# Kernel optimization log

Hardware: AMD Instinct MI355X
Metric: run time of the kernel (lower is better)

The kernel has to match this reference:

```python
import jax, jax.numpy as jnp
import numpy as np

B = 65536
BASE_CW = 0.5  # constraint weight at epoch 0 (progress=0)

def setup_inputs() -> dict:
    key = jax.random.key(0)
    k1, k2 = jax.random.split(key)
    outputs = jax.random.normal(k1, (B, 81, 9), dtype=jnp.float32)
    targets = jax.random.randint(k2, (B, 81), 0, 9, dtype=jnp.int64)
    return {"outputs": outputs, "targets": targets}

def reference(outputs, targets):
    b = outputs.shape[0]
    # log-softmax over the 9 digit classes (single stable pass)
    logp = jax.nn.log_softmax(outputs, axis=2)            # (B, 81, 9)
    t = targets.reshape(-1)                               # (B*81,)
    # cross entropy (mean over all cells)
    ce = -jnp.take_along_axis(logp.reshape(-1, 9), t[:, None], axis=1).mean()
    probs = jnp.exp(logp)                                 # softmax probs
    grid = probs.reshape(b, 9, 9, 9)                      # (B, row, col, digit)
    # all 27 constraint MSEs fused: per-digit mean over (B, 9), summed over digits
    row_sums = grid.sum(axis=2)                           # (B, 9, 9)
    col_sums = grid.sum(axis=1)                           # (B, 9, 9)
    box_sums = grid.reshape(b, 3, 3, 3, 3, 9).sum(axis=(2, 4)).reshape(b, 9, 9)
    constraint_loss = (
        jnp.mean((row_sums - 1.0) ** 2, axis=(0, 1)).sum()
        + jnp.mean((col_sums - 1.0) ** 2, axis=(0, 1)).sum()
        + jnp.mean((box_sums - 1.0) ** 2, axis=(0, 1)).sum()
    ) / 27.0
    # confidence (entropy) term, masked by targets != -1
    mask = (t != -1).astype(outputs.dtype)                # (B*81,)
    conf = -(probs.reshape(-1, 9) * logp.reshape(-1, 9)).sum(axis=1)
    conf = (conf * mask).sum() / (mask.sum() + 1e-8)
    return ce + BASE_CW * constraint_loss + 0.1 * conf
```

## Files before the change

### kernel.cpp

```cpp
#include <hip/hip_runtime.h>

#define THREADS 256
#define BPB 8

static __global__ void zero_out_kernel(float* out) { out[0] = 0.0f; }

__launch_bounds__(THREADS)
static __global__ void sudoku_loss_kernel(const float* __restrict__ outs,
                                          const int*   __restrict__ targets,
                                          float*       __restrict__ out) {
    __shared__ float P[BPB * 729];
    __shared__ float wave_sums[THREADS / 64];

    const int tid = threadIdx.x;
    const long long board0 = (long long)blockIdx.x * BPB;
    const long long fbase  = board0 * 729;

    const float4* __restrict__ src = (const float4*)(outs + fbase);
    float4* dst = (float4*)P;
    for (int i = tid; i < (BPB * 729 / 4); i += THREADS) dst[i] = src[i];
    __syncthreads();

    float acc_a = 0.0f;
    const long long cbase = board0 * 81;
    for (int cell = tid; cell < BPB * 81; cell += THREADS) {
        const int t = targets[cbase + cell];
        float* xp = &P[cell * 9];
        float x[9];
        #pragma unroll
        for (int i = 0; i < 9; ++i) x[i] = xp[i];
        float m = x[0];
        #pragma unroll
        for (int i = 1; i < 9; ++i) m = fmaxf(m, x[i]);
        float s = 0.0f, sx = 0.0f, xt = 0.0f;
        float e[9];
        #pragma unroll
        for (int i = 0; i < 9; ++i) {
            e[i] = __expf(x[i] - m);
            s += e[i];
            sx = fmaf(e[i], x[i], sx);
            xt = (i == t) ? x[i] : xt;
        }
        const float lse = m + __logf(s);
        const float inv = 1.0f / s;
        const float ce  = lse - xt;
        const float ent = lse - sx * inv;
        acc_a += ce + 0.1f * ent;
        #pragma unroll
        for (int i = 0; i < 9; ++i) xp[i] = e[i] * inv;
    }
    __syncthreads();

    float acc_c = 0.0f;
    for (int u = tid; u < BPB * 243; u += THREADS) {
        const int q    = u / 243;
        const int r    = u - q * 243;
        const int type = r / 81;
        const int rem  = r - type * 81;
        const int unit = rem / 9;
        const int d    = rem - unit * 9;
        const float* Pq = &P[q * 729 + d];
        float ssum = 0.0f;
        if (type == 0) {
            #pragma unroll
            for (int j = 0; j < 9; ++j) ssum += Pq[(unit * 9 + j) * 9];
        } else if (type == 1) {
            #pragma unroll
            for (int j = 0; j < 9; ++j) ssum += Pq[(j * 9 + unit) * 9];
        } else {
            const int br = unit / 3, bc = unit - br * 3;
            #pragma unroll
            for (int j = 0; j < 9; ++j) {
                const int jr = j / 3, jc = j - jr * 3;
                ssum += Pq[((br * 3 + jr) * 9 + (bc * 3 + jc)) * 9];
            }
        }
        const float dlt = ssum - 1.0f;
        acc_c = fmaf(dlt, dlt, acc_c);
    }

    const float SA = 1.0f / (65536.0f * 81.0f);
    const float SB = 0.5f / (27.0f * 65536.0f * 9.0f);
    float total = acc_a * SA + acc_c * SB;
    #pragma unroll
    for (int off = 32; off > 0; off >>= 1)
        total += __shfl_down(total, off, 64);
    if ((tid & 63) == 0) wave_sums[tid >> 6] = total;
    __syncthreads();
    if (tid == 0) {
        float blk = wave_sums[0] + wave_sums[1] + wave_sums[2] + wave_sums[3];
        atomicAdd(out, blk);
    }
}

extern "C" void kernel_launch(void* const* d_in, const int* in_sizes, int n_in,
                              void* d_out, int out_size, void* d_ws, size_t ws_size,
                              hipStream_t stream) {
    const float* outs    = (const float*)d_in[0];
    const int*   targets = (const int*)d_in[1];
    float*       out     = (float*)d_out;
    hipLaunchKernelGGL(zero_out_kernel, dim3(1), dim3(1), 0, stream, out);
    hipLaunchKernelGGL(sudoku_loss_kernel, dim3(65536 / BPB), dim3(THREADS), 0, stream,
                       outs, targets, out);
}
```

Measured before the change: 336.3 us.

## Read logits directly from global and pad shared prob layout for vector reads

Drops the staging copy of logits into shared memory, so each thread loads its cell's 9 logits directly from global. Probabilities are written into a padded shared layout (12 floats per cell) using float4 stores. The constraint stage is remapped so each of 216 threads owns one (board, unit) pair and sums all 9 digits with float4 loads, instead of one thread per digit doing strided scalar reads. The risks are uncoalesced global loads, since each thread reads 36 contiguous bytes at a 36-byte stride, and fewer active threads in the constraint stage.

```diff
diff --git a/kernel.cpp b/kernel.cpp
--- a/kernel.cpp
+++ b/kernel.cpp
@@ -2,6 +2,8 @@
 
 #define THREADS 256
 #define BPB 8
+#define CELLS (BPB * 81)
+#define PADW 12
 
 static __global__ void zero_out_kernel(float* out) { out[0] = 0.0f; }
 
@@ -9,26 +11,22 @@
 static __global__ void sudoku_loss_kernel(const float* __restrict__ outs,
                                           const int*   __restrict__ targets,
                                           float*       __restrict__ out) {
-    __shared__ float P[BPB * 729];
+    __shared__ float P[CELLS * PADW];
     __shared__ float wave_sums[THREADS / 64];
 
     const int tid = threadIdx.x;
     const long long board0 = (long long)blockIdx.x * BPB;
-    const long long fbase  = board0 * 729;
-
-    const float4* __restrict__ src = (const float4*)(outs + fbase);
-    float4* dst = (float4*)P;
-    for (int i = tid; i < (BPB * 729 / 4); i += THREADS) dst[i] = src[i];
-    __syncthreads();
+    const float* __restrict__ xbase = outs + board0 * 729;
+    const int*   __restrict__ tbase = targets + board0 * 81;
 
     float acc_a = 0.0f;
-    const long long cbase = board0 * 81;
-    for (int cell = tid; cell < BPB * 81; cell += THREADS) {
-        const int t = targets[cbase + cell];
-        float* xp = &P[cell * 9];
+    for (int cell = tid; cell < CELLS; cell += THREADS) {
+        const float* __restrict__ xp = xbase + cell * 9;
+        const int t = tbase[cell];
         float x[9];
         #pragma unroll
         for (int i = 0; i < 9; ++i) x[i] = xp[i];
+
         float m = x[0];
         #pragma unroll
         for (int i = 1; i < 9; ++i) m = fmaxf(m, x[i]);
@@ -43,40 +41,48 @@
         }
         const float lse = m + __logf(s);
         const float inv = 1.0f / s;
-        const float ce  = lse - xt;
-        const float ent = lse - sx * inv;
-        acc_a += ce + 0.1f * ent;
-        #pragma unroll
-        for (int i = 0; i < 9; ++i) xp[i] = e[i] * inv;
+        acc_a += (lse - xt) + 0.1f * (lse - sx * inv);
+
+        float* __restrict__ pp = &P[cell * PADW];
+        float4 p0, p1;
+        p0.x = e[0] * inv; p0.y = e[1] * inv; p0.z = e[2] * inv; p0.w = e[3] * inv;
+        p1.x = e[4] * inv; p1.y = e[5] * inv; p1.z = e[6] * inv; p1.w = e[7] * inv;
+        *(float4*)pp       = p0;
+        *(float4*)(pp + 4) = p1;
+        pp[8] = e[8] * inv;
     }
     __syncthreads();
 
     float acc_c = 0.0f;
-    for (int u = tid; u < BPB * 243; u += THREADS) {
-        const int q    = u / 243;
-        const int r    = u - q * 243;
-        const int type = r / 81;
-        const int rem  = r - type * 81;
-        const int unit = rem / 9;
-        const int d    = rem - unit * 9;
-        const float* Pq = &P[q * 729 + d];
-        float ssum = 0.0f;
-        if (type == 0) {
-            #pragma unroll
-            for (int j = 0; j < 9; ++j) ssum += Pq[(unit * 9 + j) * 9];
-        } else if (type == 1) {
-            #pragma unroll
-            for (int j = 0; j < 9; ++j) ssum += Pq[(j * 9 + unit) * 9];
-        } else {
-            const int br = unit / 3, bc = unit - br * 3;
-            #pragma unroll
-            for (int j = 0; j < 9; ++j) {
-                const int jr = j / 3, jc = j - jr * 3;
-                ssum += Pq[((br * 3 + jr) * 9 + (bc * 3 + jc)) * 9];
-            }
+    if (tid < 27 * BPB) {
+        const int q    = tid & 7;
+        const int u27  = tid >> 3;
+        const int type = u27 / 9;
+        const int unit = u27 - type * 9;
+        const int ur3  = (unit / 3) * 3;
+        const int uc3  = (unit % 3) * 3;
+        const float* __restrict__ Pq = &P[q * 81 * PADW];
+
+        float4 s03 = make_float4(0.f, 0.f, 0.f, 0.f);
+        float4 s47 = make_float4(0.f, 0.f, 0.f, 0.f);
+        float  s8  = 0.0f;
+        #pragma unroll
+        for (int j = 0; j < 9; ++j) {
+            const int crow = unit * 9 + j;
+            const int ccol = j * 9 + unit;
+            const int cbox = (ur3 + j / 3) * 9 + uc3 + (j % 3);
+            int c = (type == 0) ? crow : ((type == 1) ? ccol : cbox);
+            const float* __restrict__ cp = Pq + c * PADW;
+            const float4 a = *(const float4*)cp;
+            const float4 b = *(const float4*)(cp + 4);
+            s03.x += a.x; s03.y += a.y; s03.z += a.z; s03.w += a.w;
+            s47.x += b.x; s47.y += b.y; s47.z += b.z; s47.w += b.w;
+            s8    += cp[8];
         }
-        const float dlt = ssum - 1.0f;
-        acc_c = fmaf(dlt, dlt, acc_c);
+        float d0 = s03.x - 1.f, d1 = s03.y - 1.f, d2 = s03.z - 1.f, d3 = s03.w - 1.f;
+        float d4 = s47.x - 1.f, d5 = s47.y - 1.f, d6 = s47.z - 1.f, d7 = s47.w - 1.f;
+        float d8 = s8 - 1.f;
+        acc_c = d0*d0 + d1*d1 + d2*d2 + d3*d3 + d4*d4 + d5*d5 + d6*d6 + d7*d7 + d8*d8;
     }
 
     const float SA = 1.0f / (65536.0f * 81.0f);
```

Measured after the change: 322.0 us. -4.3%, faster.
